# Kernel tuning notes

Hardware: AMD Instinct MI355X
Metric: run time of the kernel (lower is better)

## Reference

```python
import jax, jax.numpy as jnp
import numpy as np

B, N, L = 256, 128, 2048
NF, AC, HID = 75, 3, 256
DIM, NHEAD, FPD, NWORD = 128, 8, 679, 8600


def setup_inputs() -> dict:
    key = jax.random.key(0)
    ks = iter(jax.random.split(key, 48))
    rn = lambda *s: jax.random.normal(next(ks), s, dtype=jnp.float32) * 0.05
    d = {}
    d['V'] = jax.random.normal(next(ks), (B, N, NF), dtype=jnp.float32)
    d['A'] = jax.random.uniform(next(ks), (B, AC, N, N), dtype=jnp.float32)
    d['fp'] = jax.random.uniform(next(ks), (B, FPD), dtype=jnp.float32)
    d['mol_size'] = jax.random.randint(next(ks), (B,), 1, N + 1, dtype=jnp.int32)
    d['protein_seq'] = jax.random.randint(next(ks), (B, L), 0, NWORD)
    d['label'] = jax.random.randint(next(ks), (B,), 0, 2)
    # GConv blocks (multi-channel GCN): 75->256, 256->256, 256->256
    d['gc_W1'], d['gc_b1'] = rn(AC, NF, HID), rn(HID)
    d['gc_W2'], d['gc_b2'] = rn(AC, HID, HID), rn(HID)
    d['gc_W3'], d['gc_b3'] = rn(AC, HID, HID), rn(HID)
    # fp linear chain: 679->128, 128->128
    d['fp_W1'], d['fp_b1'] = rn(FPD, DIM), rn(DIM)
    d['fp_W2'], d['fp_b2'] = rn(DIM, DIM), rn(DIM)
    # global attention pooling (per-head node scores) + readout
    d['att_W'] = rn(HID, NHEAD)
    d['ro_W'], d['ro_b'] = rn(HID * NHEAD, DIM), rn(DIM)
    d['emb'] = rn(NWORD, DIM)
    # cross-attention projections
    d['mfp_W'], d['mfp_b'] = rn(DIM, DIM), rn(DIM)
    d['pfp_W'], d['pfp_b'] = rn(DIM, DIM), rn(DIM)
    d['mv_W'], d['mv_b'] = rn(DIM, DIM), rn(DIM)
    d['pv_W'], d['pv_b'] = rn(DIM, DIM), rn(DIM)
    # stacked MLPs (3 layers each, width 2*dim)
    d['mlp1_W'], d['mlp1_b'] = rn(3, 2 * DIM, 2 * DIM), rn(3, 2 * DIM)
    d['mlp2_W'], d['mlp2_b'] = rn(3, 2 * DIM, 2 * DIM), rn(3, 2 * DIM)
    d['out1_W'], d['out1_b'] = rn(2 * DIM, 2), rn(2)
    d['out2_W'], d['out2_b'] = rn(2 * DIM, 2), rn(2)
    return d


def _gconv(V, A, W, b):
    # A: [b,c,n,m], V: [b,m,f], W: [c,f,o]
    AV = jnp.einsum('bcnm,bmf->bcnf', A, V)
    return jax.nn.relu(jnp.einsum('bcnf,cfo->bno', AV, W) + b)


def _cross_attn(hvec, prot_emb, mW, mb, pW, pb):
    # hvec: [b,d]; prot_emb: [b,l,d]
    h = jax.nn.relu(hvec @ mW + mb)                       # [b,d]
    hs = jax.nn.relu(jnp.einsum('bld,de->ble', prot_emb, pW) + pb)  # [b,l,d]
    w = jnp.tanh(jnp.einsum('bd,bld->bl', h, hs))         # [b,l]
    ys = w[..., None] * hs                                 # [b,l,d]
    return jnp.max(ys, axis=1)                             # [b,d]


def reference(V, A, fp, mol_size, protein_seq, label,
              gc_W1, gc_b1, gc_W2, gc_b2, gc_W3, gc_b3,
              fp_W1, fp_b1, fp_W2, fp_b2, att_W, ro_W, ro_b, emb,
              mfp_W, mfp_b, pfp_W, pfp_b, mv_W, mv_b, pv_W, pv_b,
              mlp1_W, mlp1_b, mlp2_W, mlp2_b, out1_W, out1_b, out2_W, out2_b):
    # fp linear chain (dropout = identity at inference)
    fp = jax.nn.relu(fp @ fp_W1 + fp_b1)
    fp = jax.nn.relu(fp @ fp_W2 + fp_b2)
    # graph conv blocks
    Vh = _gconv(V, A, gc_W1, gc_b1)
    Vh = _gconv(Vh, A, gc_W2, gc_b2)
    Vh = _gconv(Vh, A, gc_W3, gc_b3)
    # masked multi-head global attention pooling over nodes
    scores = jnp.einsum('bnf,fh->bnh', Vh, att_W)          # [b,n,heads]
    mask = jnp.arange(N)[None, :] < mol_size[:, None]       # [b,n]
    scores = jnp.where(mask[..., None], scores, -1e9)
    att = jax.nn.softmax(scores, axis=1)
    pooled = jnp.einsum('bnh,bnf->bhf', att, Vh).reshape(Vh.shape[0], -1)  # [b, heads*nf]
    Vr = jax.nn.relu(pooled @ ro_W + ro_b)                  # [b,dim]
    # protein embedding + ragged cross-attention branches
    prot_emb = emb[protein_seq]                             # [b,l,dim]
    itact1 = _cross_attn(fp, prot_emb, mfp_W, mfp_b, pfp_W, pfp_b)
    itact2 = _cross_attn(Vr, prot_emb, mv_W, mv_b, pv_W, pv_b)
    cat1 = jnp.concatenate([fp, itact1], axis=1)
    cat2 = jnp.concatenate([Vr, itact2], axis=1)
    for i in range(mlp1_W.shape[0]):
        cat1 = jax.nn.relu(cat1 @ mlp1_W[i] + mlp1_b[i])
        cat2 = jax.nn.relu(cat2 @ mlp2_W[i] + mlp2_b[i])
    pred_itact = (cat1 @ out1_W + out1_b) + (cat2 @ out2_W + out2_b)
    pred_labels = jnp.argmax(pred_itact, axis=1)
    pred_scores = jax.nn.softmax(pred_itact, axis=1)[:, 1]
    return (pred_itact, label, pred_labels, pred_scores)
```

## Files before the change

kernel.cpp:

```cpp
#include <hip/hip_runtime.h>
#include <math.h>

static constexpr int BB   = 256;
static constexpr int NN   = 128;
static constexpr int LL   = 2048;
static constexpr int NF   = 75;
static constexpr int AC   = 3;
static constexpr int HID  = 256;
static constexpr int DIM  = 128;
static constexpr int NHEAD= 8;
static constexpr int FPD  = 679;
static constexpr int FPDP = 704;
static constexpr int NWORD= 8600;
static constexpr int NWP  = 8704;
static constexpr int KB   = 768;

typedef __attribute__((ext_vector_type(8))) _Float16 f16x8;
typedef __attribute__((ext_vector_type(2))) _Float16 h2v;
typedef __attribute__((ext_vector_type(4))) float f32x4;
typedef unsigned int u32;
typedef unsigned short u16;

__device__ __forceinline__ u16 f2h(float x) {
    _Float16 h = (_Float16)x;
    return *(u16*)&h;
}
__device__ __forceinline__ u16 f2h_sat(float x) {
    x = fminf(fmaxf(x, -65000.f), 65000.f);
    _Float16 h = (_Float16)x;
    return *(u16*)&h;
}
__device__ __forceinline__ float h2f(u16 x) {
    return (float)(*(_Float16*)&x);
}

static constexpr float SC   = 0.0625f;
static constexpr float USC  = 16.0f;

__global__ __launch_bounds__(256)
void prepA_kernel(const float* __restrict__ A, u16* __restrict__ Ah)
{
    size_t base = (size_t)blockIdx.x * (NN * NN);
    int t = threadIdx.x;
    #pragma unroll
    for (int i = 0; i < 16; ++i) {
        int id = t + i * 256;
        float4 v = *(const float4*)(A + base + (size_t)id * 4);
        u32 p0 = (u32)f2h(v.x) | ((u32)f2h(v.y) << 16);
        u32 p1 = (u32)f2h(v.z) | ((u32)f2h(v.w) << 16);
        *(uint2*)(Ah + base + (size_t)id * 4) = make_uint2(p0, p1);
    }
}

__global__ __launch_bounds__(256)
void prepVt_kernel(const float* __restrict__ V, u16* __restrict__ Vt)
{
    int b = blockIdx.x, t = threadIdx.x;
    __shared__ float sV[NN * NF];
    for (int i = t; i < NN * NF; i += 256) sV[i] = V[(size_t)b * (NN * NF) + i];
    __syncthreads();
    for (int i = t; i < 80 * 128; i += 256) {
        int f = i >> 7, n = i & 127;
        float v = (f < NF) ? sV[n * NF + f] : 0.f;
        Vt[(size_t)b * (80 * 128) + i] = f2h(v);
    }
}

__global__ __launch_bounds__(256)
void prepAllW_kernel(const float* __restrict__ gcW1, const float* __restrict__ gcW2,
                     const float* __restrict__ gcW3,
                     const float* __restrict__ fpW1, const float* __restrict__ fpW2,
                     const float* __restrict__ pfpW, const float* __restrict__ pvW,
                     const float* __restrict__ mfpW, const float* __restrict__ mvW,
                     const float* __restrict__ m1W,  const float* __restrict__ m2W,
                     const float* __restrict__ fp,
                     u16* __restrict__ Wt1, u16* __restrict__ Wt2, u16* __restrict__ Wt3,
                     u16* __restrict__ W1t, u16* __restrict__ W2t,
                     u16* __restrict__ pWt12, u16* __restrict__ mWt12,
                     u16* __restrict__ Wmlp, u16* __restrict__ fph)
{
    int o = blockIdx.x, z = blockIdx.y, t = threadIdx.x;
    if (z == 0) {
        int k = t;
        int c = k / 80, f = k - c * 80;
        float v = (c < 3 && f < NF) ? gcW1[((size_t)c * NF + f) * HID + o] : 0.f;
        Wt1[(size_t)o * 256 + k] = f2h(v);
    } else if (z == 1 || z == 2) {
        const float* W = (z == 1) ? gcW2 : gcW3;
        u16* Wt = (z == 1) ? Wt2 : Wt3;
        for (int k = t; k < KB; k += 256) {
            int c = k >> 8, f = k & 255;
            Wt[(size_t)o * KB + k] = f2h(W[((size_t)c * HID + f) * HID + o]);
        }
    } else if (z == 3) {
        if (o < 128) {
            for (int k = t; k < FPDP; k += 256) {
                float v = (k < FPD) ? fpW1[(size_t)k * DIM + o] : 0.f;
                W1t[(size_t)o * FPDP + k] = f2h(v);
            }
            if (t < 128) W2t[(size_t)o * 128 + t] = f2h(fpW2[(size_t)t * DIM + o]);
        }
    } else if (z == 4) {
        if (o < 128 && t < 128) {
            pWt12[(size_t)0 * 16384 + o * 128 + t] = f2h(pfpW[(size_t)t * 128 + o]);
            pWt12[(size_t)1 * 16384 + o * 128 + t] = f2h(pvW [(size_t)t * 128 + o]);
            mWt12[(size_t)0 * 16384 + o * 128 + t] = f2h(mfpW[(size_t)t * 128 + o]);
            mWt12[(size_t)1 * 16384 + o * 128 + t] = f2h(mvW [(size_t)t * 128 + o]);
        }
    } else if (z == 5 || z == 6) {
        int br = z - 5;
        const float* W = br ? m2W : m1W;
        #pragma unroll
        for (int Lr = 0; Lr < 3; ++Lr)
            Wmlp[(((size_t)(br * 3 + Lr)) * 256 + o) * 256 + t] =
                f2h(W[(size_t)Lr * 256 * 256 + (size_t)t * 256 + o]);
    } else {
        for (int i = t; i < FPDP; i += 256) {
            float v = (i < FPD) ? fp[(size_t)o * FPD + i] : 0.f;
            fph[(size_t)o * FPDP + i] = f2h(v);
        }
    }
}

__global__ __launch_bounds__(256)
void fp12_mfma(const u16* __restrict__ fph, const u16* __restrict__ W1t,
               const float* __restrict__ b1, const u16* __restrict__ W2t,
               const float* __restrict__ b2, float* __restrict__ FP2,
               u16* __restrict__ FP2h)
{
    __shared__ u16 As[128 * 40];
    __shared__ u16 Bs[128 * 40];
    __shared__ u16 Xs[128 * 136];
    int mt = blockIdx.x;
    const u16* Ap = fph + (size_t)(mt * 128) * FPDP;

    int t = threadIdx.x;
    int l = t & 63, wid = t >> 6;
    int rb = (wid >> 1) * 64, cb = (wid & 1) * 64;
    int ln = l & 15, q = l >> 4;

    {
        f32x4 acc[4][4] = {};
        for (int kt = 0; kt < FPDP / 32; ++kt) {
            #pragma unroll
            for (int i = 0; i < 2; ++i) {
                int id = t + i * 256;
                int row = id >> 2, qh = id & 3;
                *(uint4*)&As[row * 40 + qh * 8] =
                    *(const uint4*)(Ap + (size_t)row * FPDP + kt * 32 + qh * 8);
                *(uint4*)&Bs[row * 40 + qh * 8] =
                    *(const uint4*)(W1t + (size_t)row * FPDP + kt * 32 + qh * 8);
            }
            __syncthreads();
            f16x8 af[4], bfr[4];
            #pragma unroll
            for (int fr = 0; fr < 4; ++fr)
                af[fr] = *(const f16x8*)&As[(rb + fr * 16 + ln) * 40 + q * 8];
            #pragma unroll
            for (int fc = 0; fc < 4; ++fc)
                bfr[fc] = *(const f16x8*)&Bs[(cb + fc * 16 + ln) * 40 + q * 8];
            #pragma unroll
            for (int fr = 0; fr < 4; ++fr)
                #pragma unroll
                for (int fc = 0; fc < 4; ++fc)
                    acc[fr][fc] = __builtin_amdgcn_mfma_f32_16x16x32_f16(
                        af[fr], bfr[fc], acc[fr][fc], 0, 0, 0);
            __syncthreads();
        }
        #pragma unroll
        for (int fr = 0; fr < 4; ++fr)
            #pragma unroll
            for (int fc = 0; fc < 4; ++fc) {
                int d = cb + fc * 16 + ln;
                float bv = b1[d];
                #pragma unroll
                for (int r = 0; r < 4; ++r) {
                    int m = rb + fr * 16 + q * 4 + r;
                    Xs[m * 136 + d] = f2h(fmaxf(acc[fr][fc][r] + bv, 0.f));
                }
            }
    }
    f32x4 acc[4][4] = {};
    for (int kt = 0; kt < 4; ++kt) {
        __syncthreads();
        #pragma unroll
        for (int i = 0; i < 2; ++i) {
            int id = t + i * 256;
            int row = id >> 2, qh = id & 3;
            *(uint4*)&Bs[row * 40 + qh * 8] =
                *(const uint4*)(W2t + (size_t)row * 128 + kt * 32 + qh * 8);
        }
        __syncthreads();
        f16x8 af[4], bfr[4];
        #pragma unroll
        for (int fr = 0; fr < 4; ++fr)
            af[fr] = *(const f16x8*)&Xs[(rb + fr * 16 + ln) * 136 + kt * 32 + q * 8];
        #pragma unroll
        for (int fc = 0; fc < 4; ++fc)
            bfr[fc] = *(const f16x8*)&Bs[(cb + fc * 16 + ln) * 40 + q * 8];
        #pragma unroll
        for (int fr = 0; fr < 4; ++fr)
            #pragma unroll
            for (int fc = 0; fc < 4; ++fc)
                acc[fr][fc] = __builtin_amdgcn_mfma_f32_16x16x32_f16(
                    af[fr], bfr[fc], acc[fr][fc], 0, 0, 0);
    }
    #pragma unroll
    for (int fr = 0; fr < 4; ++fr)
        #pragma unroll
        for (int fc = 0; fc < 4; ++fc) {
            int d = cb + fc * 16 + ln;
            float bv = b2[d];
            #pragma unroll
            for (int r = 0; r < 4; ++r) {
                int m = rb + fr * 16 + q * 4 + r;
                float val = fmaxf(acc[fr][fc][r] + bv, 0.f);
                FP2 [(size_t)(mt * 128 + m) * 128 + d] = val;
                FP2h[(size_t)(mt * 128 + m) * 128 + d] = f2h(val);
            }
        }
}

__global__ __launch_bounds__(256)
void hs12_mfma(const float* __restrict__ emb, const u16* __restrict__ pWt12,
               const float* __restrict__ ba, const float* __restrict__ bb_,
               u16* __restrict__ HS12)
{
    __shared__ u16 As[128 * 40];
    __shared__ u16 Bs[128 * 40];
    int ft = blockIdx.x, br = blockIdx.y;
    const u16* Bp = pWt12 + (size_t)br * 128 * 128;
    const float* bias = br ? bb_ : ba;
    int r0 = ft * 128;

    int t = threadIdx.x;
    int l = t & 63, wid = t >> 6;
    int rb = (wid >> 1) * 64, cb = (wid & 1) * 64;
    int ln = l & 15, q = l >> 4;

    f32x4 acc[4][4] = {};

    for (int kt = 0; kt < 4; ++kt) {
        #pragma unroll
        for (int i = 0; i < 4; ++i) {
            int id = t + i * 256;
            int row = id >> 3, qf = id & 7;
            int r = r0 + row;
            float4 v = make_float4(0.f, 0.f, 0.f, 0.f);
            if (r < NWORD) v = *(const float4*)(emb + (size_t)r * 128 + kt * 32 + qf * 4);
            u32 p0 = (u32)f2h(v.x) | ((u32)f2h(v.y) << 16);
            u32 p1 = (u32)f2h(v.z) | ((u32)f2h(v.w) << 16);
            u32* dst = (u32*)&As[row * 40 + qf * 4];
            dst[0] = p0; dst[1] = p1;
        }
        #pragma unroll
        for (int i = 0; i < 2; ++i) {
            int id = t + i * 256;
            int row = id >> 2, qh = id & 3;
            *(uint4*)&Bs[row * 40 + qh * 8] =
                *(const uint4*)(Bp + (size_t)row * 128 + kt * 32 + qh * 8);
        }
        __syncthreads();
        f16x8 af[4], bfr[4];
        #pragma unroll
        for (int fr = 0; fr < 4; ++fr)
            af[fr] = *(const f16x8*)&As[(rb + fr * 16 + ln) * 40 + q * 8];
        #pragma unroll
        for (int fc = 0; fc < 4; ++fc)
            bfr[fc] = *(const f16x8*)&Bs[(cb + fc * 16 + ln) * 40 + q * 8];
        #pragma unroll
        for (int fr = 0; fr < 4; ++fr)
            #pragma unroll
            for (int fc = 0; fc < 4; ++fc)
                acc[fr][fc] = __builtin_amdgcn_mfma_f32_16x16x32_f16(
                    af[fr], bfr[fc], acc[fr][fc], 0, 0, 0);
        __syncthreads();
    }
    #pragma unroll
    for (int fr = 0; fr < 4; ++fr)
        #pragma unroll
        for (int fc = 0; fc < 4; ++fc) {
            int d = cb + fc * 16 + ln;
            float bv = bias[d];
            #pragma unroll
            for (int r = 0; r < 4; ++r) {
                int m = rb + fr * 16 + q * 4 + r;
                int rr = r0 + m;
                if (rr < NWORD)
                    HS12[(size_t)rr * 256 + br * 128 + d] = f2h(fmaxf(acc[fr][fc][r] + bv, 0.f));
            }
        }
}

__global__ __launch_bounds__(256)
void gA_mfma(const u16* __restrict__ Agr, const u16* __restrict__ Htr,
             u16* __restrict__ AV, int b0, int htStride, int fpMul, int Fvalid)
{
    __shared__ u16 As[128 * 40];
    __shared__ u16 Bs[128 * 40];
    int ft = blockIdx.x, c = blockIdx.y, bl = blockIdx.z;
    int b = b0 + bl;
    const u16* Ap = Agr + ((size_t)b * AC + c) * (NN * NN);
    const u16* Bp = Htr + (size_t)b * htStride + ft * (128 * 128);
    u16* Cp = AV + (size_t)bl * (NN * KB) + c * fpMul + ft * 128;

    int t = threadIdx.x;
    int l = t & 63, wid = t >> 6;
    int rb = (wid >> 1) * 64, cb = (wid & 1) * 64;
    int ln = l & 15, q = l >> 4;

    f32x4 acc[4][4] = {};

    for (int kt = 0; kt < 4; ++kt) {
        #pragma unroll
        for (int i = 0; i < 2; ++i) {
            int id = t + i * 256;
            int row = id >> 2, qh = id & 3;
            *(uint4*)&As[row * 40 + qh * 8] =
                *(const uint4*)(Ap + (size_t)row * NN + kt * 32 + qh * 8);
        }
        #pragma unroll
        for (int i = 0; i < 2; ++i) {
            int id = t + i * 256;
            int row = id >> 2, qh = id & 3;
            uint4 v = make_uint4(0, 0, 0, 0);
            if (row < Fvalid) v = *(const uint4*)(Bp + (size_t)row * 128 + kt * 32 + qh * 8);
            *(uint4*)&Bs[row * 40 + qh * 8] = v;
        }
        __syncthreads();
        f16x8 af[4], bfr[4];
        #pragma unroll
        for (int fr = 0; fr < 4; ++fr)
            af[fr] = *(const f16x8*)&As[(rb + fr * 16 + ln) * 40 + q * 8];
        #pragma unroll
        for (int fc = 0; fc < 4; ++fc)
            bfr[fc] = *(const f16x8*)&Bs[(cb + fc * 16 + ln) * 40 + q * 8];
        #pragma unroll
        for (int fr = 0; fr < 4; ++fr)
            #pragma unroll
            for (int fc = 0; fc < 4; ++fc)
                acc[fr][fc] = __builtin_amdgcn_mfma_f32_16x16x32_f16(
                    af[fr], bfr[fc], acc[fr][fc], 0, 0, 0);
        __syncthreads();
    }
    #pragma unroll
    for (int fr = 0; fr < 4; ++fr) {
        #pragma unroll
        for (int fc = 0; fc < 4; ++fc) {
            int fcol = cb + fc * 16 + ln;
            if (fcol < Fvalid) {
                #pragma unroll
                for (int r = 0; r < 4; ++r) {
                    int n = rb + fr * 16 + q * 4 + r;
                    Cp[(size_t)n * KB + fcol] = f2h_sat(acc[fr][fc][r] * SC);
                }
            }
        }
    }
}

__global__ __launch_bounds__(256)
void gA2_mfma(const u16* __restrict__ Agr, const u16* __restrict__ Htr,
              u16* __restrict__ AV, int b0)
{
    __shared__ u16 As[4][128 * 40];
    __shared__ u16 Bs[128 * 40];
    int c = blockIdx.x, bl = blockIdx.y;
    int b = b0 + bl;
    const u16* Ap = Agr + ((size_t)b * AC + c) * (NN * NN);
    u16* Cp0 = AV + (size_t)bl * (NN * KB) + c * 256;

    int t = threadIdx.x;
    int l = t & 63, wid = t >> 6;
    int rb = (wid >> 1) * 64, cb = (wid & 1) * 64;
    int ln = l & 15, q = l >> 4;

    #pragma unroll
    for (int i = 0; i < 8; ++i) {
        int id = t + i * 256;
        int row = id >> 4, kq = id & 15;
        int kt = kq >> 2, qh = kq & 3;
        *(uint4*)&As[kt][row * 40 + qh * 8] =
            *(const uint4*)(Ap + (size_t)row * NN + kt * 32 + qh * 8);
    }

    for (int ft = 0; ft < 2; ++ft) {
        const u16* Bp = Htr + (size_t)b * (HID * NN) + ft * (128 * 128);
        f32x4 acc[4][4] = {};
        for (int kt = 0; kt < 4; ++kt) {
            __syncthreads();
            #pragma unroll
            for (int i = 0; i < 2; ++i) {
                int id = t + i * 256;
                int row = id >> 2, qh = id & 3;
                *(uint4*)&Bs[row * 40 + qh * 8] =
                    *(const uint4*)(Bp + (size_t)row * 128 + kt * 32 + qh * 8);
            }
            __syncthreads();
            f16x8 af[4], bfr[4];
            #pragma unroll
            for (int fr = 0; fr < 4; ++fr)
                af[fr] = *(const f16x8*)&As[kt][(rb + fr * 16 + ln) * 40 + q * 8];
            #pragma unroll
            for (int fc = 0; fc < 4; ++fc)
                bfr[fc] = *(const f16x8*)&Bs[(cb + fc * 16 + ln) * 40 + q * 8];
            #pragma unroll
            for (int fr = 0; fr < 4; ++fr)
                #pragma unroll
                for (int fc = 0; fc < 4; ++fc)
                    acc[fr][fc] = __builtin_amdgcn_mfma_f32_16x16x32_f16(
                        af[fr], bfr[fc], acc[fr][fc], 0, 0, 0);
        }
        #pragma unroll
        for (int fr = 0; fr < 4; ++fr)
            #pragma unroll
            for (int fc = 0; fc < 4; ++fc) {
                int fcol = ft * 128 + cb + fc * 16 + ln;
                #pragma unroll
                for (int r = 0; r < 4; ++r) {
                    int n = rb + fr * 16 + q * 4 + r;
                    Cp0[(size_t)n * KB + fcol] = f2h_sat(acc[fr][fc][r] * SC);
                }
            }
    }
}

__global__ __launch_bounds__(256)
void gB_mfma(const u16* __restrict__ AV, const u16* __restrict__ Wt,
             const float* __restrict__ bias, u16* __restrict__ Hout,
             int b0, int kTiles, int Ks, int mode)
{
    __shared__ u16 As[128 * 40];
    __shared__ u16 Bs[128 * 40];
    int ot = blockIdx.x, bl = blockIdx.y;
    int b = b0 + bl;
    const u16* Ap = AV + (size_t)bl * (NN * KB);
    const u16* Bp = Wt + (size_t)ot * 128 * Ks;

    int t = threadIdx.x;
    int l = t & 63, wid = t >> 6;
    int rb = (wid >> 1) * 64, cb = (wid & 1) * 64;
    int ln = l & 15, q = l >> 4;

    f32x4 acc[4][4] = {};

    for (int kt = 0; kt < kTiles; ++kt) {
        #pragma unroll
        for (int i = 0; i < 2; ++i) {
            int id = t + i * 256;
            int row = id >> 2, qh = id & 3;
            *(uint4*)&As[row * 40 + qh * 8] =
                *(const uint4*)(Ap + (size_t)row * KB + kt * 32 + qh * 8);
            *(uint4*)&Bs[row * 40 + qh * 8] =
                *(const uint4*)(Bp + (size_t)row * Ks + kt * 32 + qh * 8);
        }
        __syncthreads();
        f16x8 af[4], bfr[4];
        #pragma unroll
        for (int fr = 0; fr < 4; ++fr)
            af[fr] = *(const f16x8*)&As[(rb + fr * 16 + ln) * 40 + q * 8];
        #pragma unroll
        for (int fc = 0; fc < 4; ++fc)
            bfr[fc] = *(const f16x8*)&Bs[(cb + fc * 16 + ln) * 40 + q * 8];
        #pragma unroll
        for (int fr = 0; fr < 4; ++fr)
            #pragma unroll
            for (int fc = 0; fc < 4; ++fc)
                acc[fr][fc] = __builtin_amdgcn_mfma_f32_16x16x32_f16(
                    af[fr], bfr[fc], acc[fr][fc], 0, 0, 0);
        __syncthreads();
    }
    if (mode == 0) {
        #pragma unroll
        for (int fr = 0; fr < 4; ++fr)
            #pragma unroll
            for (int fc = 0; fc < 4; ++fc) {
                int oc = cb + fc * 16 + ln;
                float bv = bias[ot * 128 + oc];
                int n0 = rb + fr * 16 + q * 4;
                u16 v0 = f2h_sat(fmaxf(acc[fr][fc][0] * USC + bv, 0.f));
                u16 v1 = f2h_sat(fmaxf(acc[fr][fc][1] * USC + bv, 0.f));
                u16 v2 = f2h_sat(fmaxf(acc[fr][fc][2] * USC + bv, 0.f));
                u16 v3 = f2h_sat(fmaxf(acc[fr][fc][3] * USC + bv, 0.f));
                uint2 pk = make_uint2((u32)v0 | ((u32)v1 << 16),
                                      (u32)v2 | ((u32)v3 << 16));
                *(uint2*)(Hout + ((size_t)b * HID + ot * 128 + oc) * NN + n0) = pk;
            }
    } else {
        #pragma unroll
        for (int fr = 0; fr < 4; ++fr)
            #pragma unroll
            for (int fc = 0; fc < 4; ++fc) {
                int oc = cb + fc * 16 + ln;
                float bv = bias[ot * 128 + oc];
                #pragma unroll
                for (int r = 0; r < 4; ++r) {
                    int n = rb + fr * 16 + q * 4 + r;
                    float val = fmaxf(acc[fr][fc][r] * USC + bv, 0.f);
                    Hout[((size_t)b * NN + n) * HID + ot * 128 + oc] = f2h_sat(val * SC);
                }
            }
    }
}

__global__ __launch_bounds__(256)
void pool_kernel(const u16* __restrict__ H3h,
                 const float* __restrict__ attW,
                 const int* __restrict__ msz,
                 float* __restrict__ pooled)
{
    int b = blockIdx.x, t = threadIdx.x;
    __shared__ u16  sTh[128][264];
    __shared__ float sW[HID * NHEAD];
    __shared__ float sS[NN * NHEAD];
    __shared__ float sP[16][NHEAD][2];
    for (int i = t; i < HID * NHEAD; i += 256) sW[i] = attW[i];
    const u16* Hb = H3h + (size_t)b * NN * HID;
    for (int i = t; i < 128 * 32; i += 256) {
        int row = i >> 5, fq = (i & 31) * 8;
        *(uint4*)&sTh[row][fq] = *(const uint4*)(Hb + (size_t)row * HID + fq);
    }
    __syncthreads();
    for (int n0 = 0; n0 < NN; n0 += 16) {
        int nl = t >> 4, h = (t >> 1) & 7, fh = t & 1;
        float s = 0.f;
        for (int f = fh * 128; f < fh * 128 + 128; ++f)
            s += h2f(sTh[n0 + nl][f]) * sW[f * NHEAD + h];
        sP[nl][h][fh] = s;
        __syncthreads();
        if (t < 128) {
            int n2 = t >> 3, h2 = t & 7;
            sS[(n0 + n2) * NHEAD + h2] = USC * (sP[n2][h2][0] + sP[n2][h2][1]);
        }
        __syncthreads();
    }
    int ms = msz[b];
    int h = t >> 5, ln = t & 31;
    float mx = -1e9f;
    for (int n = ln; n < NN; n += 32) {
        float s = (n < ms) ? sS[n * NHEAD + h] : -1e9f;
        mx = fmaxf(mx, s);
    }
    #pragma unroll
    for (int off = 16; off; off >>= 1) mx = fmaxf(mx, __shfl_xor(mx, off, 32));
    float sum = 0.f;
    for (int n = ln; n < NN; n += 32) {
        float s = (n < ms) ? sS[n * NHEAD + h] : -1e9f;
        sum += expf(s - mx);
    }
    #pragma unroll
    for (int off = 16; off; off >>= 1) sum += __shfl_xor(sum, off, 32);
    float inv = 1.f / sum;
    for (int n = ln; n < NN; n += 32) {
        float s = (n < ms) ? sS[n * NHEAD + h] : -1e9f;
        sS[n * NHEAD + h] = expf(s - mx) * inv;
    }
    __syncthreads();
    float accp[NHEAD] = {};
    for (int n = 0; n < NN; ++n) {
        float hv = h2f(sTh[n][t]);
        #pragma unroll
        for (int hh = 0; hh < NHEAD; ++hh) accp[hh] += sS[n * NHEAD + hh] * hv;
    }
    #pragma unroll
    for (int hh = 0; hh < NHEAD; ++hh)
        pooled[(size_t)b * (HID * NHEAD) + hh * HID + t] = USC * accp[hh];
}

__global__ __launch_bounds__(128)
void readout_part(const float* __restrict__ pooled,
                  const float* __restrict__ roW,
                  float* __restrict__ Rp)
{
    int b = blockIdx.x, s = blockIdx.y, t = threadIdx.x;
    __shared__ float sx[256];
    const float* sp = pooled + (size_t)b * (HID * NHEAD) + s * 256;
    sx[t] = sp[t];
    sx[t + 128] = sp[t + 128];
    __syncthreads();
    float acc = 0.f;
    const float* W = roW + (size_t)(s * 256) * DIM + t;
    for (int k = 0; k < 256; ++k) acc += sx[k] * W[(size_t)k * DIM];
    Rp[((size_t)s * BB + b) * DIM + t] = acc;
}

__global__ __launch_bounds__(128)
void readout_merge(const float* __restrict__ Rp,
                   const float* __restrict__ rob,
                   float* __restrict__ Vr, u16* __restrict__ Vrh)
{
    int b = blockIdx.x, t = threadIdx.x;
    float a = rob[t];
    #pragma unroll
    for (int s = 0; s < 8; ++s) a += Rp[((size_t)s * BB + b) * DIM + t];
    float v = fmaxf(a, 0.f);
    Vr [(size_t)b * DIM + t] = v;
    Vrh[(size_t)b * DIM + t] = f2h_sat(v * SC);
}

__global__ __launch_bounds__(256)
void atth_mfma(const u16* __restrict__ FP2h, const u16* __restrict__ VRh,
               const u16* __restrict__ mWt12,
               const float* __restrict__ mfpb, const float* __restrict__ mvb,
               u16* __restrict__ h1h, u16* __restrict__ h2h)
{
    __shared__ u16 As[128 * 40];
    __shared__ u16 Bs[128 * 40];
    int mt = blockIdx.x, br = blockIdx.y;
    const u16* Ap = (br ? VRh : FP2h) + (size_t)(mt * 128) * 128;
    const u16* Bp = mWt12 + (size_t)br * 128 * 128;
    const float* bias = br ? mvb : mfpb;
    float unsc = br ? USC : 1.f;
    u16* out = br ? h2h : h1h;

    int t = threadIdx.x;
    int l = t & 63, wid = t >> 6;
    int rb = (wid >> 1) * 64, cb = (wid & 1) * 64;
    int ln = l & 15, q = l >> 4;

    f32x4 acc[4][4] = {};

    for (int kt = 0; kt < 4; ++kt) {
        #pragma unroll
        for (int i = 0; i < 2; ++i) {
            int id = t + i * 256;
            int row = id >> 2, qh = id & 3;
            *(uint4*)&As[row * 40 + qh * 8] =
                *(const uint4*)(Ap + (size_t)row * 128 + kt * 32 + qh * 8);
            *(uint4*)&Bs[row * 40 + qh * 8] =
                *(const uint4*)(Bp + (size_t)row * 128 + kt * 32 + qh * 8);
        }
        __syncthreads();
        f16x8 af[4], bfr[4];
        #pragma unroll
        for (int fr = 0; fr < 4; ++fr)
            af[fr] = *(const f16x8*)&As[(rb + fr * 16 + ln) * 40 + q * 8];
        #pragma unroll
        for (int fc = 0; fc < 4; ++fc)
            bfr[fc] = *(const f16x8*)&Bs[(cb + fc * 16 + ln) * 40 + q * 8];
        #pragma unroll
        for (int fr = 0; fr < 4; ++fr)
            #pragma unroll
            for (int fc = 0; fc < 4; ++fc)
                acc[fr][fc] = __builtin_amdgcn_mfma_f32_16x16x32_f16(
                    af[fr], bfr[fc], acc[fr][fc], 0, 0, 0);
        __syncthreads();
    }
    #pragma unroll
    for (int fr = 0; fr < 4; ++fr)
        #pragma unroll
        for (int fc = 0; fc < 4; ++fc) {
            int d = cb + fc * 16 + ln;
            float bv = bias[d];
            #pragma unroll
            for (int r = 0; r < 4; ++r) {
                int m = rb + fr * 16 + q * 4 + r;
                out[(size_t)(mt * 128 + m) * 128 + d] =
                    f2h_sat(fmaxf(acc[fr][fc][r] * unsc + bv, 0.f));
            }
        }
}

__global__ __launch_bounds__(256)
void cross_part_kernel(const int* __restrict__ seq,
                       const u16* __restrict__ HS12,
                       const u16* __restrict__ h1h, const u16* __restrict__ h2h,
                       float* __restrict__ Pc)
{
    int b = blockIdx.x, s = blockIdx.y, t = threadIdx.x;
    int g = t >> 4, gl = t & 15;
    int d0 = gl * 8;
    f16x8 h1 = *(const f16x8*)(h1h + (size_t)b * DIM + d0);
    f16x8 h2 = *(const f16x8*)(h2h + (size_t)b * DIM + d0);
    const h2v* h1p = (const h2v*)&h1;
    const h2v* h2p = (const h2v*)&h2;
    h2v m1[4], m2[4];
    _Float16 NEGBIG = (_Float16)(-65504.f);
    #pragma unroll
    for (int k = 0; k < 4; ++k) { m1[k] = (h2v){NEGBIG, NEGBIG}; m2[k] = (h2v){NEGBIG, NEGBIG}; }
    const int* sq = seq + (size_t)b * LL + s * 256;
    for (int it = 0; it < 16; ++it) {
        int tok = sq[g + 16 * it];
        const u16* r12 = HS12 + (size_t)tok * 256 + d0;
        f16x8 va = *(const f16x8*)(r12);
        f16x8 vb = *(const f16x8*)(r12 + 128);
        const h2v* vap = (const h2v*)&va;
        const h2v* vbp = (const h2v*)&vb;
        float p1 = 0.f, p2 = 0.f;
        #pragma unroll
        for (int k = 0; k < 4; ++k) {
            p1 = __builtin_amdgcn_fdot2(vap[k], h1p[k], p1, false);
            p2 = __builtin_amdgcn_fdot2(vbp[k], h2p[k], p2, false);
        }
        #pragma unroll
        for (int off = 8; off; off >>= 1) {
            p1 += __shfl_xor(p1, off);
            p2 += __shfl_xor(p2, off);
        }
        float w1 = 1.f - 2.f / (__expf(2.f * p1) + 1.f);
        float w2 = 1.f - 2.f / (__expf(2.f * p2) + 1.f);
        _Float16 w1s = (_Float16)w1, w2s = (_Float16)w2;
        h2v w1p = (h2v){w1s, w1s}, w2p = (h2v){w2s, w2s};
        #pragma unroll
        for (int k = 0; k < 4; ++k) {
            h2v pr1 = w1p * vap[k];
            h2v pr2 = w2p * vbp[k];
            m1[k] = (h2v){ m1[k][0] > pr1[0] ? m1[k][0] : pr1[0],
                           m1[k][1] > pr1[1] ? m1[k][1] : pr1[1] };
            m2[k] = (h2v){ m2[k][0] > pr2[0] ? m2[k][0] : pr2[0],
                           m2[k][1] > pr2[1] ? m2[k][1] : pr2[1] };
        }
    }
    __shared__ float red[16][2][DIM];
    #pragma unroll
    for (int k = 0; k < 4; ++k) {
        red[g][0][d0 + 2 * k]     = (float)m1[k][0];
        red[g][0][d0 + 2 * k + 1] = (float)m1[k][1];
        red[g][1][d0 + 2 * k]     = (float)m2[k][0];
        red[g][1][d0 + 2 * k + 1] = (float)m2[k][1];
    }
    __syncthreads();
    int tb = t >> 7, d = t & 127;
    float mx = red[0][tb][d];
    #pragma unroll
    for (int gg = 1; gg < 16; ++gg) mx = fmaxf(mx, red[gg][tb][d]);
    Pc[(((size_t)s * BB + b) * 2 + tb) * DIM + d] = mx;
}

__global__ __launch_bounds__(256)
void mlp3_mfma(const float* __restrict__ FP2, const float* __restrict__ VR,
               const float* __restrict__ Pc, const u16* __restrict__ Wmlp,
               const float* __restrict__ m1b, const float* __restrict__ m2b,
               u16* __restrict__ Yf)
{
    __shared__ u16 XY[2][128 * 264];
    __shared__ u16 Bs[128 * 40];
    int mt = blockIdx.x, br = blockIdx.y;
    int t = threadIdx.x;

    for (int i = t; i < 128 * 256; i += 256) {
        int row = i >> 8, col = i & 255;
        int b = mt * 128 + row;
        float v;
        if (col < 128) {
            v = (br ? VR : FP2)[(size_t)b * 128 + col];
        } else {
            int d = col - 128;
            float m = -INFINITY;
            #pragma unroll
            for (int s = 0; s < 8; ++s)
                m = fmaxf(m, Pc[(((size_t)s * BB + b) * 2 + br) * DIM + d]);
            v = m;
        }
        XY[0][row * 264 + col] = f2h_sat(v * SC);
    }

    int l = t & 63, wid = t >> 6;
    int rb = (wid >> 1) * 64, cb = (wid & 1) * 64;
    int ln = l & 15, q = l >> 4;

    int cur = 0;
    for (int Lr = 0; Lr < 3; ++Lr) {
        const float* bias = (br ? m2b : m1b) + (size_t)Lr * 256;
        for (int ot = 0; ot < 2; ++ot) {
            const u16* Bp = Wmlp + (((size_t)(br * 3 + Lr)) * 256 + ot * 128) * 256;
            f32x4 acc[4][4] = {};
            for (int kt = 0; kt < 8; ++kt) {
                __syncthreads();
                #pragma unroll
                for (int i = 0; i < 2; ++i) {
                    int id = t + i * 256;
                    int row = id >> 2, qh = id & 3;
                    *(uint4*)&Bs[row * 40 + qh * 8] =
                        *(const uint4*)(Bp + (size_t)row * 256 + kt * 32 + qh * 8);
                }
                __syncthreads();
                f16x8 af[4], bfr[4];
                #pragma unroll
                for (int fr = 0; fr < 4; ++fr)
                    af[fr] = *(const f16x8*)&XY[cur][(rb + fr * 16 + ln) * 264 + kt * 32 + q * 8];
                #pragma unroll
                for (int fc = 0; fc < 4; ++fc)
                    bfr[fc] = *(const f16x8*)&Bs[(cb + fc * 16 + ln) * 40 + q * 8];
                #pragma unroll
                for (int fr = 0; fr < 4; ++fr)
                    #pragma unroll
                    for (int fc = 0; fc < 4; ++fc)
                        acc[fr][fc] = __builtin_amdgcn_mfma_f32_16x16x32_f16(
                            af[fr], bfr[fc], acc[fr][fc], 0, 0, 0);
            }
            #pragma unroll
            for (int fr = 0; fr < 4; ++fr)
                #pragma unroll
                for (int fc = 0; fc < 4; ++fc) {
                    int oc = cb + fc * 16 + ln;
                    float bv = bias[ot * 128 + oc] * SC;
                    #pragma unroll
                    for (int r = 0; r < 4; ++r) {
                        int m = rb + fr * 16 + q * 4 + r;
                        XY[cur ^ 1][m * 264 + ot * 128 + oc] =
                            f2h_sat(fmaxf(acc[fr][fc][r] + bv, 0.f));
                    }
                }
        }
        cur ^= 1;
    }
    __syncthreads();
    for (int i = t; i < 128 * 32; i += 256) {
        int row = i >> 5, c8 = (i & 31) * 8;
        *(uint4*)(Yf + ((size_t)br * BB + mt * 128 + row) * 256 + c8) =
            *(const uint4*)&XY[cur][row * 264 + c8];
    }
}

__global__ __launch_bounds__(256)
void mlp_out_kernel(const u16* __restrict__ Y,
                    const float* __restrict__ o1W, const float* __restrict__ o1b,
                    const float* __restrict__ o2W, const float* __restrict__ o2b,
                    const int* __restrict__ label,
                    float* __restrict__ dout)
{
    int b = blockIdx.x, t = threadIdx.x;
    __shared__ float pl[2][128];
    const u16* y1 = Y + (size_t)b * 256;
    const u16* y2 = Y + ((size_t)BB + b) * 256;
    int j = t & 1, k2 = t >> 1;
    float p = USC * (h2f(y1[k2])       * o1W[k2 * 2 + j]
                   + h2f(y1[k2 + 128]) * o1W[(k2 + 128) * 2 + j]
                   + h2f(y2[k2])       * o2W[k2 * 2 + j]
                   + h2f(y2[k2 + 128]) * o2W[(k2 + 128) * 2 + j]);
    pl[j][k2] = p;
    __syncthreads();
    for (int s = 64; s > 0; s >>= 1) {
        if (k2 < s) pl[j][k2] += pl[j][k2 + s];
        __syncthreads();
    }
    if (t == 0) {
        float l0 = pl[0][0] + o1b[0] + o2b[0];
        float l1 = pl[1][0] + o1b[1] + o2b[1];
        dout[(size_t)b * 2 + 0] = l0;
        dout[(size_t)b * 2 + 1] = l1;
        dout[2 * BB + b] = (float)label[b];
        dout[3 * BB + b] = (float)((l1 > l0) ? 1 : 0);
        float mx = fmaxf(l0, l1);
        float e0 = expf(l0 - mx), e1 = expf(l1 - mx);
        dout[4 * BB + b] = e1 / (e0 + e1);
    }
}

extern "C" void kernel_launch(void* const* d_in, const int* in_sizes, int n_in,
                              void* d_out, int out_size, void* d_ws, size_t ws_size,
                              hipStream_t stream)
{
    const float* V    = (const float*)d_in[0];
    const float* A    = (const float*)d_in[1];
    const float* fp   = (const float*)d_in[2];
    const int*   msz  = (const int*)  d_in[3];
    const int*   seq  = (const int*)  d_in[4];
    const int*   lab  = (const int*)  d_in[5];
    const float* gcW1 = (const float*)d_in[6];  const float* gcb1 = (const float*)d_in[7];
    const float* gcW2 = (const float*)d_in[8];  const float* gcb2 = (const float*)d_in[9];
    const float* gcW3 = (const float*)d_in[10]; const float* gcb3 = (const float*)d_in[11];
    const float* fpW1 = (const float*)d_in[12]; const float* fpb1 = (const float*)d_in[13];
    const float* fpW2 = (const float*)d_in[14]; const float* fpb2 = (const float*)d_in[15];
    const float* attW = (const float*)d_in[16];
    const float* roW  = (const float*)d_in[17]; const float* rob  = (const float*)d_in[18];
    const float* emb  = (const float*)d_in[19];
    const float* mfpW = (const float*)d_in[20]; const float* mfpb = (const float*)d_in[21];
    const float* pfpW = (const float*)d_in[22]; const float* pfpb = (const float*)d_in[23];
    const float* mvW  = (const float*)d_in[24]; const float* mvb  = (const float*)d_in[25];
    const float* pvW  = (const float*)d_in[26]; const float* pvb  = (const float*)d_in[27];
    const float* m1W  = (const float*)d_in[28]; const float* m1b  = (const float*)d_in[29];
    const float* m2W  = (const float*)d_in[30]; const float* m2b  = (const float*)d_in[31];
    const float* o1W  = (const float*)d_in[32]; const float* o1b  = (const float*)d_in[33];
    const float* o2W  = (const float*)d_in[34]; const float* o2b  = (const float*)d_in[35];
    float* dout = (float*)d_out;

    char* ws = (char*)d_ws;
    size_t off = 0;
    auto alloc = [&](size_t bytes) -> char* {
        char* p = ws + off;
        off += (bytes + 255) & ~(size_t)255;
        return p;
    };
    u16*   Ah    = (u16*)  alloc((size_t)BB * AC * NN * NN * 2);
    u16*   Vt    = (u16*)  alloc((size_t)BB * 80 * 128 * 2);
    u16*   Wt1   = (u16*)  alloc((size_t)256 * 256 * 2);
    u16*   Wt2   = (u16*)  alloc((size_t)256 * KB * 2);
    u16*   Wt3   = (u16*)  alloc((size_t)256 * KB * 2);
    u16*   Ht    = (u16*)  alloc((size_t)BB * HID * NN * 2);
    u16*   H3h   = (u16*)  alloc((size_t)BB * NN * HID * 2);
    u16*   fph   = (u16*)  alloc((size_t)BB * FPDP * 2);
    u16*   W1t   = (u16*)  alloc((size_t)DIM * FPDP * 2);
    u16*   W2t   = (u16*)  alloc((size_t)DIM * DIM * 2);
    float* FP2   = (float*)alloc((size_t)BB * DIM * 4);
    u16*   FP2h  = (u16*)  alloc((size_t)BB * DIM * 2);
    u16*   pWt12 = (u16*)  alloc((size_t)2 * 128 * 128 * 2);
    u16*   mWt12 = (u16*)  alloc((size_t)2 * 128 * 128 * 2);
    u16*   HS12  = (u16*)  alloc((size_t)NWP * 256 * 2);
    float* PO    = (float*)alloc((size_t)BB * HID * NHEAD * 4);
    float* VR    = (float*)alloc((size_t)BB * DIM * 4);
    u16*   VRh   = (u16*)  alloc((size_t)BB * DIM * 2);
    u16*   h1h   = (u16*)  alloc((size_t)BB * DIM * 2);
    u16*   h2h   = (u16*)  alloc((size_t)BB * DIM * 2);
    float* Pc    = (float*)alloc((size_t)8 * BB * 2 * DIM * 4);
    float* Rp    = (float*)alloc((size_t)8 * BB * DIM * 4);
    u16*   Wmlp  = (u16*)  alloc((size_t)2 * 3 * 256 * 256 * 2);
    u16*   Yf    = (u16*)  alloc((size_t)2 * BB * 256 * 2);
    size_t fixedBytes = off;

    int CB = 8;
    size_t perB = (size_t)NN * KB * 2;
    {
        const int tiers[] = {256, 128, 64, 32, 16, 8, 4, 2, 1};
        for (int i = 0; i < 9; ++i)
            if (fixedBytes + (size_t)tiers[i] * perB <= ws_size) { CB = tiers[i]; break; }
    }
    u16* AV = (u16*)(ws + fixedBytes);

    prepA_kernel<<<BB * AC, 256, 0, stream>>>(A, Ah);
    prepVt_kernel<<<BB, 256, 0, stream>>>(V, Vt);
    prepAllW_kernel<<<dim3(256, 8), 256, 0, stream>>>(
        gcW1, gcW2, gcW3, fpW1, fpW2, pfpW, pvW, mfpW, mvW, m1W, m2W, fp,
        Wt1, Wt2, Wt3, W1t, W2t, pWt12, mWt12, Wmlp, fph);
    fp12_mfma<<<2, 256, 0, stream>>>(fph, W1t, fpb1, W2t, fpb2, FP2, FP2h);
    hs12_mfma<<<dim3(NWP / 128, 2), 256, 0, stream>>>(emb, pWt12, pfpb, pvb, HS12);

    for (int b0 = 0; b0 < BB; b0 += CB) {
        gA_mfma<<<dim3(1, AC, CB), 256, 0, stream>>>(Ah, Vt, AV, b0, 80 * 128, 80, 80);
        gB_mfma<<<dim3(2, CB), 256, 0, stream>>>(AV, Wt1, gcb1, Ht, b0, 8, 256, 0);
    }
    for (int b0 = 0; b0 < BB; b0 += CB) {
        gA2_mfma<<<dim3(AC, CB), 256, 0, stream>>>(Ah, Ht, AV, b0);
        gB_mfma<<<dim3(2, CB), 256, 0, stream>>>(AV, Wt2, gcb2, Ht, b0, 24, KB, 0);
    }
    for (int b0 = 0; b0 < BB; b0 += CB) {
        gA2_mfma<<<dim3(AC, CB), 256, 0, stream>>>(Ah, Ht, AV, b0);
        gB_mfma<<<dim3(2, CB), 256, 0, stream>>>(AV, Wt3, gcb3, H3h, b0, 24, KB, 1);
    }

    pool_kernel<<<BB, 256, 0, stream>>>(H3h, attW, msz, PO);
    readout_part<<<dim3(BB, 8), 128, 0, stream>>>(PO, roW, Rp);
    readout_merge<<<BB, 128, 0, stream>>>(Rp, rob, VR, VRh);
    atth_mfma<<<dim3(2, 2), 256, 0, stream>>>(FP2h, VRh, mWt12, mfpb, mvb, h1h, h2h);
    cross_part_kernel<<<dim3(BB, 8), 256, 0, stream>>>(seq, HS12, h1h, h2h, Pc);
    mlp3_mfma<<<dim3(2, 2), 256, 0, stream>>>(FP2, VR, Pc, Wmlp, m1b, m2b, Yf);
    mlp_out_kernel<<<BB, 256, 0, stream>>>(Yf, o1W, o1b, o2W, o2b, lab, dout);
}
```

Before: 521.8 us.

## Split fused 3-layer MLP kernel into per-layer launches with more blocks

The single 4-block kernel that ran all three MLP layers in shared memory is replaced by a small input-prep kernel and three per-layer GEMM launches of 8 blocks each, with output tiles split across blocks. The goal is more parallelism across compute units for this tail stage and a cheaper, parallel input gather. In exchange it adds several kernel launches and round-trips of intermediate activations through global memory.

```diff
diff --git a/kernel.cpp b/kernel.cpp
--- a/kernel.cpp
+++ b/kernel.cpp
@@ -728,89 +728,82 @@
 }
 
 __global__ __launch_bounds__(256)
-void mlp3_mfma(const float* __restrict__ FP2, const float* __restrict__ VR,
-               const float* __restrict__ Pc, const u16* __restrict__ Wmlp,
+void prepX_kernel(const float* __restrict__ FP2, const float* __restrict__ VR,
+                  const float* __restrict__ Pc, u16* __restrict__ Xh)
+{
+    int b = blockIdx.x, br = blockIdx.y, t = threadIdx.x;
+    float v;
+    if (t < 128) {
+        v = (br ? VR : FP2)[(size_t)b * 128 + t];
+    } else {
+        int d = t - 128;
+        float m = -INFINITY;
+        #pragma unroll
+        for (int s = 0; s < 8; ++s)
+            m = fmaxf(m, Pc[(((size_t)s * BB + b) * 2 + br) * DIM + d]);
+        v = m;
+    }
+    Xh[((size_t)br * BB + b) * 256 + t] = f2h_sat(v * SC);
+}
+
+__global__ __launch_bounds__(256)
+void mlpL_mfma(const u16* __restrict__ X, const u16* __restrict__ Wmlp,
                const float* __restrict__ m1b, const float* __restrict__ m2b,
-               u16* __restrict__ Yf)
-{
-    __shared__ u16 XY[2][128 * 264];
+               int Lr, u16* __restrict__ Y)
+{
+    __shared__ u16 As[128 * 40];
     __shared__ u16 Bs[128 * 40];
-    int mt = blockIdx.x, br = blockIdx.y;
+    int mt = blockIdx.x, ot = blockIdx.y, br = blockIdx.z;
+    const u16* Ap = X + ((size_t)br * BB + mt * 128) * 256;
+    const u16* Bp = Wmlp + (((size_t)(br * 3 + Lr)) * 256 + ot * 128) * 256;
+    const float* bias = (br ? m2b : m1b) + (size_t)Lr * 256 + ot * 128;
+
     int t = threadIdx.x;
-
-    for (int i = t; i < 128 * 256; i += 256) {
-        int row = i >> 8, col = i & 255;
-        int b = mt * 128 + row;
-        float v;
-        if (col < 128) {
-            v = (br ? VR : FP2)[(size_t)b * 128 + col];
-        } else {
-            int d = col - 128;
-            float m = -INFINITY;
-            #pragma unroll
-            for (int s = 0; s < 8; ++s)
-                m = fmaxf(m, Pc[(((size_t)s * BB + b) * 2 + br) * DIM + d]);
-            v = m;
-        }
-        XY[0][row * 264 + col] = f2h_sat(v * SC);
-    }
-
     int l = t & 63, wid = t >> 6;
     int rb = (wid >> 1) * 64, cb = (wid & 1) * 64;
     int ln = l & 15, q = l >> 4;
 
-    int cur = 0;
-    for (int Lr = 0; Lr < 3; ++Lr) {
-        const float* bias = (br ? m2b : m1b) + (size_t)Lr * 256;
-        for (int ot = 0; ot < 2; ++ot) {
-            const u16* Bp = Wmlp + (((size_t)(br * 3 + Lr)) * 256 + ot * 128) * 256;
-            f32x4 acc[4][4] = {};
-            for (int kt = 0; kt < 8; ++kt) {
-                __syncthreads();
-                #pragma unroll
-                for (int i = 0; i < 2; ++i) {
-                    int id = t + i * 256;
-                    int row = id >> 2, qh = id & 3;
-                    *(uint4*)&Bs[row * 40 + qh * 8] =
-                        *(const uint4*)(Bp + (size_t)row * 256 + kt * 32 + qh * 8);
-                }
-                __syncthreads();
-                f16x8 af[4], bfr[4];
-                #pragma unroll
-                for (int fr = 0; fr < 4; ++fr)
-                    af[fr] = *(const f16x8*)&XY[cur][(rb + fr * 16 + ln) * 264 + kt * 32 + q * 8];
-                #pragma unroll
-                for (int fc = 0; fc < 4; ++fc)
-                    bfr[fc] = *(const f16x8*)&Bs[(cb + fc * 16 + ln) * 40 + q * 8];
-                #pragma unroll
-                for (int fr = 0; fr < 4; ++fr)
-                    #pragma unroll
-                    for (int fc = 0; fc < 4; ++fc)
-                        acc[fr][fc] = __builtin_amdgcn_mfma_f32_16x16x32_f16(
-                            af[fr], bfr[fc], acc[fr][fc], 0, 0, 0);
-            }
-            #pragma unroll
-            for (int fr = 0; fr < 4; ++fr)
-                #pragma unroll
-                for (int fc = 0; fc < 4; ++fc) {
-                    int oc = cb + fc * 16 + ln;
-                    float bv = bias[ot * 128 + oc] * SC;
-                    #pragma unroll
-                    for (int r = 0; r < 4; ++r) {
-                        int m = rb + fr * 16 + q * 4 + r;
-                        XY[cur ^ 1][m * 264 + ot * 128 + oc] =
-                            f2h_sat(fmaxf(acc[fr][fc][r] + bv, 0.f));
-                    }
-                }
-        }
-        cur ^= 1;
-    }
-    __syncthreads();
-    for (int i = t; i < 128 * 32; i += 256) {
-        int row = i >> 5, c8 = (i & 31) * 8;
-        *(uint4*)(Yf + ((size_t)br * BB + mt * 128 + row) * 256 + c8) =
-            *(const uint4*)&XY[cur][row * 264 + c8];
-    }
+    f32x4 acc[4][4] = {};
+
+    for (int kt = 0; kt < 8; ++kt) {
+        #pragma unroll
+        for (int i = 0; i < 2; ++i) {
+            int id = t + i * 256;
+            int row = id >> 2, qh = id & 3;
+            *(uint4*)&As[row * 40 + qh * 8] =
+                *(const uint4*)(Ap + (size_t)row * 256 + kt * 32 + qh * 8);
+            *(uint4*)&Bs[row * 40 + qh * 8] =
+                *(const uint4*)(Bp + (size_t)row * 256 + kt * 32 + qh * 8);
+        }
+        __syncthreads();
+        f16x8 af[4], bfr[4];
+        #pragma unroll
+        for (int fr = 0; fr < 4; ++fr)
+            af[fr] = *(const f16x8*)&As[(rb + fr * 16 + ln) * 40 + q * 8];
+        #pragma unroll
+        for (int fc = 0; fc < 4; ++fc)
+            bfr[fc] = *(const f16x8*)&Bs[(cb + fc * 16 + ln) * 40 + q * 8];
+        #pragma unroll
+        for (int fr = 0; fr < 4; ++fr)
+            #pragma unroll
+            for (int fc = 0; fc < 4; ++fc)
+                acc[fr][fc] = __builtin_amdgcn_mfma_f32_16x16x32_f16(
+                    af[fr], bfr[fc], acc[fr][fc], 0, 0, 0);
+        __syncthreads();
+    }
+    #pragma unroll
+    for (int fr = 0; fr < 4; ++fr)
+        #pragma unroll
+        for (int fc = 0; fc < 4; ++fc) {
+            int oc = cb + fc * 16 + ln;
+            float bv = bias[oc] * SC;
+            #pragma unroll
+            for (int r = 0; r < 4; ++r) {
+                int m = rb + fr * 16 + q * 4 + r;
+                Y[((size_t)br * BB + (mt * 128 + m)) * 256 + ot * 128 + oc] =
+                    f2h_sat(fmaxf(acc[fr][fc][r] + bv, 0.f));
+            }
+        }
 }
 
 __global__ __launch_bounds__(256)
@@ -906,7 +899,8 @@
     float* Pc    = (float*)alloc((size_t)8 * BB * 2 * DIM * 4);
     float* Rp    = (float*)alloc((size_t)8 * BB * DIM * 4);
     u16*   Wmlp  = (u16*)  alloc((size_t)2 * 3 * 256 * 256 * 2);
-    u16*   Yf    = (u16*)  alloc((size_t)2 * BB * 256 * 2);
+    u16*   Xa    = (u16*)  alloc((size_t)2 * BB * 256 * 2);
+    u16*   Xb    = (u16*)  alloc((size_t)2 * BB * 256 * 2);
     size_t fixedBytes = off;
 
     int CB = 8;
@@ -944,6 +938,9 @@
     readout_merge<<<BB, 128, 0, stream>>>(Rp, rob, VR, VRh);
     atth_mfma<<<dim3(2, 2), 256, 0, stream>>>(FP2h, VRh, mWt12, mfpb, mvb, h1h, h2h);
     cross_part_kernel<<<dim3(BB, 8), 256, 0, stream>>>(seq, HS12, h1h, h2h, Pc);
-    mlp3_mfma<<<dim3(2, 2), 256, 0, stream>>>(FP2, VR, Pc, Wmlp, m1b, m2b, Yf);
-    mlp_out_kernel<<<BB, 256, 0, stream>>>(Yf, o1W, o1b, o2W, o2b, lab, dout);
-}
+    prepX_kernel<<<dim3(BB, 2), 256, 0, stream>>>(FP2, VR, Pc, Xa);
+    mlpL_mfma<<<dim3(2, 2, 2), 256, 0, stream>>>(Xa, Wmlp, m1b, m2b, 0, Xb);
+    mlpL_mfma<<<dim3(2, 2, 2), 256, 0, stream>>>(Xb, Wmlp, m1b, m2b, 1, Xa);
+    mlpL_mfma<<<dim3(2, 2, 2), 256, 0, stream>>>(Xa, Wmlp, m1b, m2b, 2, Xb);
+    mlp_out_kernel<<<BB, 256, 0, stream>>>(Xb, o1W, o1b, o2W, o2b, lab, dout);
+}
```

Measured after the change: 472.8 us. -9.4%, faster.
